# Performance work log

Measured on AMD Instinct MI355X. Metric: run time of the kernel, lower is better.

The kernel has to match this reference:

```python
import jax, jax.numpy as jnp
import numpy as np

W, H = 256, 256          # image width (x) and height (y); image indexed [x, y] like the torch code
N = 8192                 # depth-sorted visible gaussians
TILE = 16                # tile_size default
CHUNK = 128              # gaussians composited per scan step (N % CHUNK == 0)
MIN_WEIGHT = 1e-6        # early-termination threshold from render_pixel


def setup_inputs() -> dict:
    key = jax.random.key(0)
    k1, k2, k3, k4, k5 = jax.random.split(key, 5)
    # pixel-space means, uniformly over the image
    points_xy = jax.random.uniform(k1, (N, 2), dtype=jnp.float32) * jnp.array([W, H], jnp.float32)
    # SPD inverse 2D covariances: Sigma = R diag(var) R^T, inv = R diag(1/var) R^T
    theta = jax.random.uniform(k2, (N,), dtype=jnp.float32) * (2.0 * np.pi)
    sig = jax.random.uniform(k3, (N, 2), dtype=jnp.float32, minval=1.5, maxval=8.0)
    var = sig ** 2
    ct, st = jnp.cos(theta), jnp.sin(theta)
    R = jnp.stack([jnp.stack([ct, -st], -1), jnp.stack([st, ct], -1)], -2)  # [N,2,2]
    inverse_covariance = jnp.einsum('nij,nj,nkj->nik', R, 1.0 / var, R)
    # radius = ceil(2.5 * sqrt(max eigenvalue)) as in compute_radius
    radius = jnp.ceil(2.5 * jnp.sqrt(jnp.max(var, axis=1)))
    colors = jax.random.uniform(k4, (N, 3), dtype=jnp.float32)
    opacity = jax.random.normal(k5, (N,), dtype=jnp.float32)  # pre-sigmoid logits
    return dict(points_xy=points_xy, inverse_covariance=inverse_covariance,
                radius=radius, colors=colors, opacity=opacity)


def _rasterize(points_xy, inverse_covariance, radius, colors, opacity):
    px = jnp.arange(W, dtype=jnp.float32)[:, None]   # [W,1] pixel x coords
    py = jnp.arange(H, dtype=jnp.float32)[None, :]   # [1,H] pixel y coords
    # tile origin for each pixel (tile-based culling as in render_image)
    tile_x0 = ((jnp.arange(W) // TILE) * TILE).astype(jnp.float32)[:, None]  # [W,1]
    tile_y0 = ((jnp.arange(H) // TILE) * TILE).astype(jnp.float32)[None, :]  # [1,H]
    # per-gaussian bounding boxes (preprocess)
    min_x = jnp.floor(points_xy[:, 0] - radius); max_x = jnp.ceil(points_xy[:, 0] + radius)
    min_y = jnp.floor(points_xy[:, 1] - radius); max_y = jnp.ceil(points_xy[:, 1] + radius)

    n_chunks = N // CHUNK
    def chunk(a):
        return a.reshape((n_chunks, CHUNK) + a.shape[1:])
    xs = dict(mx=chunk(points_xy[:, 0]), my=chunk(points_xy[:, 1]),
              a=chunk(inverse_covariance[:, 0, 0]), b=chunk(inverse_covariance[:, 0, 1]),
              c=chunk(inverse_covariance[:, 1, 1]),
              mnx=chunk(min_x), mxx=chunk(max_x), mny=chunk(min_y), mxy=chunk(max_y),
              col=chunk(colors), op=chunk(opacity))

    @jax.checkpoint
    def body(carry, ch):
        T, color = carry  # T: [W,H] remaining transmittance; color: [W,H,3]
        dx = px[None] - ch['mx'][:, None, None]  # [C,W,1]
        dy = py[None] - ch['my'][:, None, None]  # [C,1,H]
        # mahalanobis form d^T Sigma^{-1} d with symmetric inv cov [[a,b],[b,c]]
        q = (ch['a'][:, None, None] * dx * dx
             + 2.0 * ch['b'][:, None, None] * dx * dy
             + ch['c'][:, None, None] * dy * dy)              # [C,W,H]
        alpha = jnp.exp(-0.5 * q) * jax.nn.sigmoid(ch['op'])[:, None, None]
        # gaussian participates for a pixel iff its bbox intersects that pixel's tile
        in_tile = ((ch['mnx'][:, None, None] <= tile_x0[None] + TILE)
                   & (ch['mxx'][:, None, None] >= tile_x0[None])
                   & (ch['mny'][:, None, None] <= tile_y0[None] + TILE)
                   & (ch['mxy'][:, None, None] >= tile_y0[None]))   # [C,W,H]
        alpha = jnp.where(in_tile, alpha, 0.0)
        cum = jnp.cumprod(1.0 - alpha, axis=0)                 # inclusive prefix of (1-alpha)
        T_before = T[None] * jnp.concatenate([jnp.ones_like(cum[:1]), cum[:-1]], axis=0)
        # original: test_weight = T_before*(1-alpha); terminate (skip contribution) if < min_weight
        include = (T[None] * cum) >= MIN_WEIGHT
        contrib = jnp.where(include, T_before * alpha, 0.0)   # [C,W,H]
        color = color + jnp.einsum('cwh,cd->whd', contrib, ch['col'])
        return (T * cum[-1], color), None

    init = (jnp.ones((W, H), jnp.float32), jnp.zeros((W, H, 3), jnp.float32))
    (_, color), _ = jax.lax.scan(body, init, xs)
    return color  # [W,H,3] image indexed [x,y]


def reference(points_xy, inverse_covariance, radius, colors, opacity):
    return _rasterize(points_xy, inverse_covariance, radius, colors, opacity)
```

## Files before the change

### kernel.cpp

```cpp
#include <hip/hip_runtime.h>
#include <hip/hip_fp16.h>

#define WIDTH   256
#define HEIGHT  256
#define NG      8192
#define TILE_SZ 16
#define MINW    1e-6f
#define BLK     1024
#define NBATCH  (NG / BLK)
#define NWAVE   (BLK / 64)
#define NSEG    16
#define RSZ     512
#define KC      (-0.72134752044f)

__global__ __launch_bounds__(256) void prep_kernel(
    const float* __restrict__ pts, const float* __restrict__ icov,
    const float* __restrict__ cols, const float* __restrict__ opac,
    const float* __restrict__ rad,
    float4* __restrict__ table, float4* __restrict__ bbt)
{
    const int g = blockIdx.x * 256 + threadIdx.x;
    const float2 p = ((const float2*)pts)[g];
    const float4 ic = ((const float4*)icov)[g];
    const float r  = rad[g];
    const float op = 1.0f / (1.0f + __expf(-opac[g]));
    const __half2 h = __floats2half2_rn(cols[3 * g], cols[3 * g + 1]);
    unsigned rgbits; __builtin_memcpy(&rgbits, &h, 4);
    table[2 * g + 0] = make_float4(p.x, p.y, KC * ic.x, 2.0f * KC * ic.y);
    table[2 * g + 1] = make_float4(KC * ic.w, op, __uint_as_float(rgbits),
                                   cols[3 * g + 2]);
    bbt[g] = make_float4(floorf(p.x - r), ceilf(p.x + r),
                         floorf(p.y - r), ceilf(p.y + r));
}

__global__ __launch_bounds__(BLK, 4) void raster_kernel(
    const float4* __restrict__ bbt,
    const float4* __restrict__ table,
    float* __restrict__ out)
{
    __shared__ unsigned long long s_ball[NBATCH * NWAVE];
    __shared__ int s_pfx[NBATCH * NWAVE];
    __shared__ __align__(16) char s_pool[32768];
    unsigned short* s_list = (unsigned short*)s_pool;
    float4* s_g = (float4*)(s_pool + 16384);
    __shared__ float s_P[NSEG][256];

    const int tid  = threadIdx.x;
    const int lane = tid & 63;
    const int wave = tid >> 6;
    const int seg  = wave;
    const float tx0 = (float)(blockIdx.x * TILE_SZ);
    const float ty0 = (float)(blockIdx.y * TILE_SZ);
    const float tx1 = tx0 + (float)TILE_SZ;
    const float ty1 = ty0 + (float)TILE_SZ;

    float4 bb[NBATCH];
    #pragma unroll
    for (int b = 0; b < NBATCH; ++b) bb[b] = bbt[b * BLK + tid];
    unsigned int hitbits = 0;
    #pragma unroll
    for (int b = 0; b < NBATCH; ++b) {
        bool hit = (bb[b].x <= tx1) & (bb[b].y >= tx0)
                 & (bb[b].z <= ty1) & (bb[b].w >= ty0);
        unsigned long long m = __ballot(hit);
        if (lane == 0) s_ball[b * NWAVE + wave] = m;
        if (hit) hitbits |= (1u << b);
    }
    __syncthreads();
    if (wave == 0) {
        int v0 = __popcll(s_ball[lane]);
        int v1 = __popcll(s_ball[64 + lane]);
        #pragma unroll
        for (int d = 1; d < 64; d <<= 1) {
            const int t0 = __shfl_up(v0, d);
            const int t1 = __shfl_up(v1, d);
            if (lane >= d) { v0 += t0; v1 += t1; }
        }
        s_pfx[lane] = v0;
        s_pfx[64 + lane] = v1 + __shfl(v0, 63);
    }
    __syncthreads();
    const int count = s_pfx[127];
    {
        unsigned int hb = hitbits;
        const unsigned long long ltmask = (1ull << lane) - 1ull;
        while (hb) {
            const int b = __ffs(hb) - 1;  hb &= hb - 1;
            const int idx = b * NWAVE + wave;
            const unsigned long long m = s_ball[idx];
            const int bs = idx ? s_pfx[idx - 1] : 0;
            s_list[bs + __popcll(m & ltmask)] = (unsigned short)(b * BLK + tid);
        }
    }
    __syncthreads();

    const int q  = tid & 63;
    const int qx = q >> 3, qy = q & 7;
    const float fx = tx0 + (float)(2 * qx);
    const float fy = ty0 + (float)(2 * qy);
    const int p0 = (2 * qx) * 16 + 2 * qy;
    const int pxi[4] = {p0, p0 + 1, p0 + 16, p0 + 17};
    float Tpx = 1.0f;
    float acc[3][4];
    #pragma unroll
    for (int c = 0; c < 3; ++c)
        #pragma unroll
        for (int k = 0; k < 4; ++k) acc[c][k] = 0.0f;

    for (int base = 0; base < count; base += RSZ) {
        const int n = min(RSZ, count - base);
        if (tid < n) {
            const int g = s_list[base + tid];
            s_g[tid * 2 + 0] = table[2 * g + 0];
            s_g[tid * 2 + 1] = table[2 * g + 1];
        }
        __syncthreads();

        const int L  = (n + NSEG - 1) >> 4;
        const int i0 = seg * L;
        const int i1 = min(i0 + L, n);

        float P[4] = {1.f, 1.f, 1.f, 1.f};
        float l[3][4];
        #pragma unroll
        for (int c = 0; c < 3; ++c)
            #pragma unroll
            for (int k = 0; k < 4; ++k) l[c][k] = 0.0f;

        #pragma unroll 2
        for (int i = i0; i < i1; ++i) {
            const float4 g0 = s_g[i * 2 + 0];
            const float4 g1 = s_g[i * 2 + 1];
            const float dya = fy - g0.y,  dyb = dya + 1.0f;
            const float dxa = fx - g0.x,  dxb = dxa + 1.0f;
            const float bya = g0.w * dya, byb = g0.w * dyb;
            const float cya = (g1.x * dya) * dya, cyb = (g1.x * dyb) * dyb;
            const float axa = (g0.z * dxa) * dxa, axb = (g0.z * dxb) * dxb;
            const unsigned rgbits = __float_as_uint(g1.z);
            __half2 h; __builtin_memcpy(&h, &rgbits, 4);
            const float2 rg = __half22float2(h);
            const float qv[4] = { fmaf(dxa, bya, axa + cya),
                                  fmaf(dxa, byb, axa + cyb),
                                  fmaf(dxb, bya, axb + cya),
                                  fmaf(dxb, byb, axb + cyb) };
            #pragma unroll
            for (int k = 0; k < 4; ++k) {
                const float a = g1.y * __builtin_amdgcn_exp2f(qv[k]);
                const float w = P[k] * a;
                l[0][k] = fmaf(w, rg.x, l[0][k]);
                l[1][k] = fmaf(w, rg.y, l[1][k]);
                l[2][k] = fmaf(w, g1.w, l[2][k]);
                P[k] = fmaf(-a, P[k], P[k]);
            }
        }
        #pragma unroll
        for (int k = 0; k < 4; ++k) s_P[seg][pxi[k]] = P[k];
        __syncthreads();

        if (tid < 256) {
            float run = Tpx;
            #pragma unroll
            for (int s = 0; s < NSEG; ++s) {
                const float Pv = s_P[s][tid];
                s_P[s][tid] = run;
                run *= Pv;
            }
            Tpx = run;
        }
        __syncthreads();

        float Tin[4];
        bool gated[4]; bool anyg = false;
        #pragma unroll
        for (int k = 0; k < 4; ++k) {
            Tin[k] = s_P[seg][pxi[k]];
            const bool alive = (Tin[k] >= MINW);
            gated[k] = alive && (Tin[k] * P[k] < MINW);
            if (alive && !gated[k]) {
                acc[0][k] = fmaf(Tin[k], l[0][k], acc[0][k]);
                acc[1][k] = fmaf(Tin[k], l[1][k], acc[1][k]);
                acc[2][k] = fmaf(Tin[k], l[2][k], acc[2][k]);
            }
            anyg |= gated[k];
        }
        if (__ballot(anyg) != 0ull) {
            float Tl[4] = {Tin[0], Tin[1], Tin[2], Tin[3]};
            for (int i = i0; i < i1; ++i) {
                const float4 g0 = s_g[i * 2 + 0];
                const float4 g1 = s_g[i * 2 + 1];
                const float dya = fy - g0.y,  dyb = dya + 1.0f;
                const float dxa = fx - g0.x,  dxb = dxa + 1.0f;
                const float bya = g0.w * dya, byb = g0.w * dyb;
                const float cya = (g1.x * dya) * dya, cyb = (g1.x * dyb) * dyb;
                const float axa = (g0.z * dxa) * dxa, axb = (g0.z * dxb) * dxb;
                const unsigned rgbits = __float_as_uint(g1.z);
                __half2 h; __builtin_memcpy(&h, &rgbits, 4);
                const float2 rg = __half22float2(h);
                const float qv[4] = { fmaf(dxa, bya, axa + cya),
                                      fmaf(dxa, byb, axa + cyb),
                                      fmaf(dxb, bya, axb + cya),
                                      fmaf(dxb, byb, axb + cyb) };
                #pragma unroll
                for (int k = 0; k < 4; ++k) {
                    const float a  = g1.y * __builtin_amdgcn_exp2f(qv[k]);
                    const float Tn = Tl[k] * (1.0f - a);
                    const float w  = (gated[k] && Tn >= MINW) ? Tl[k] * a : 0.0f;
                    acc[0][k] = fmaf(w, rg.x, acc[0][k]);
                    acc[1][k] = fmaf(w, rg.y, acc[1][k]);
                    acc[2][k] = fmaf(w, g1.w, acc[2][k]);
                    Tl[k] = Tn;
                }
            }
        }
        const bool mydead = (tid < 256) ? (Tpx < MINW) : true;
        if (__syncthreads_count(mydead) == BLK) break;
    }

    float sum[3];
    #pragma unroll
    for (int c = 0; c < 3; ++c) {
        __syncthreads();
        #pragma unroll
        for (int k = 0; k < 4; ++k) s_P[seg][pxi[k]] = acc[c][k];
        __syncthreads();
        if (tid < 256) {
            float v = 0.0f;
            #pragma unroll
            for (int s = 0; s < NSEG; ++s) v += s_P[s][tid];
            sum[c] = v;
        }
    }
    if (tid < 256) {
        const int x = blockIdx.x * TILE_SZ + (tid >> 4);
        const int y = blockIdx.y * TILE_SZ + (tid & 15);
        const int o = (x * HEIGHT + y) * 3;
        out[o] = sum[0];  out[o + 1] = sum[1];  out[o + 2] = sum[2];
    }
}

extern "C" void kernel_launch(void* const* d_in, const int* in_sizes, int n_in,
                              void* d_out, int out_size, void* d_ws, size_t ws_size,
                              hipStream_t stream) {
    const float* pts  = (const float*)d_in[0];
    const float* icov = (const float*)d_in[1];
    const float* rad  = (const float*)d_in[2];
    const float* cols = (const float*)d_in[3];
    const float* opac = (const float*)d_in[4];
    float* out = (float*)d_out;
    float4* table = (float4*)d_ws;
    float4* bbt   = table + 2 * NG;
    prep_kernel<<<NG / 256, 256, 0, stream>>>(pts, icov, cols, opac, rad, table, bbt);
    dim3 grid(WIDTH / TILE_SZ, HEIGHT / TILE_SZ);
    raster_kernel<<<grid, dim3(BLK), 0, stream>>>(bbt, table, out);
}
```

Baseline: 78.37 us.

## Fuse prep into raster kernel and split each tile across two blocks

Removes the separate preprocessing kernel: bounding boxes and per-gaussian parameters are now computed directly from the raw inputs inside the raster kernel, saving one launch and the workspace round-trip. Each 16x16 tile is split into two 8x16 halves via a z grid dimension, so each thread handles 2 pixels instead of 4, which doubles the block count and should give more parallelism. The final reduction writes interleaved RGB through shared memory. In exchange, culling and the per-gaussian sigmoid/fp16 packing are recomputed redundantly in every block, twice as many blocks as before.

```diff
diff --git a/kernel.cpp b/kernel.cpp
--- a/kernel.cpp
+++ b/kernel.cpp
@@ -10,32 +10,16 @@
 #define NBATCH  (NG / BLK)
 #define NWAVE   (BLK / 64)
 #define NSEG    16
+#define PXB     128
 #define RSZ     512
 #define KC      (-0.72134752044f)
 
-__global__ __launch_bounds__(256) void prep_kernel(
-    const float* __restrict__ pts, const float* __restrict__ icov,
-    const float* __restrict__ cols, const float* __restrict__ opac,
+__global__ __launch_bounds__(BLK, 8) void raster_kernel(
+    const float* __restrict__ pts,
+    const float* __restrict__ icov,
     const float* __restrict__ rad,
-    float4* __restrict__ table, float4* __restrict__ bbt)
-{
-    const int g = blockIdx.x * 256 + threadIdx.x;
-    const float2 p = ((const float2*)pts)[g];
-    const float4 ic = ((const float4*)icov)[g];
-    const float r  = rad[g];
-    const float op = 1.0f / (1.0f + __expf(-opac[g]));
-    const __half2 h = __floats2half2_rn(cols[3 * g], cols[3 * g + 1]);
-    unsigned rgbits; __builtin_memcpy(&rgbits, &h, 4);
-    table[2 * g + 0] = make_float4(p.x, p.y, KC * ic.x, 2.0f * KC * ic.y);
-    table[2 * g + 1] = make_float4(KC * ic.w, op, __uint_as_float(rgbits),
-                                   cols[3 * g + 2]);
-    bbt[g] = make_float4(floorf(p.x - r), ceilf(p.x + r),
-                         floorf(p.y - r), ceilf(p.y + r));
-}
-
-__global__ __launch_bounds__(BLK, 4) void raster_kernel(
-    const float4* __restrict__ bbt,
-    const float4* __restrict__ table,
+    const float* __restrict__ cols,
+    const float* __restrict__ opac,
     float* __restrict__ out)
 {
     __shared__ unsigned long long s_ball[NBATCH * NWAVE];
@@ -43,7 +27,8 @@
     __shared__ __align__(16) char s_pool[32768];
     unsigned short* s_list = (unsigned short*)s_pool;
     float4* s_g = (float4*)(s_pool + 16384);
-    __shared__ float s_P[NSEG][256];
+    float*  s_red = (float*)s_pool;
+    __shared__ float s_P[NSEG][PXB];
 
     const int tid  = threadIdx.x;
     const int lane = tid & 63;
@@ -54,14 +39,14 @@
     const float tx1 = tx0 + (float)TILE_SZ;
     const float ty1 = ty0 + (float)TILE_SZ;
 
-    float4 bb[NBATCH];
-    #pragma unroll
-    for (int b = 0; b < NBATCH; ++b) bb[b] = bbt[b * BLK + tid];
     unsigned int hitbits = 0;
     #pragma unroll
     for (int b = 0; b < NBATCH; ++b) {
-        bool hit = (bb[b].x <= tx1) & (bb[b].y >= tx0)
-                 & (bb[b].z <= ty1) & (bb[b].w >= ty0);
+        const int g = b * BLK + tid;
+        const float2 p = ((const float2*)pts)[g];
+        const float  r = rad[g];
+        bool hit = (floorf(p.x - r) <= tx1) & (ceilf(p.x + r) >= tx0)
+                 & (floorf(p.y - r) <= ty1) & (ceilf(p.y + r) >= ty0);
         unsigned long long m = __ballot(hit);
         if (lane == 0) s_ball[b * NWAVE + wave] = m;
         if (hit) hitbits |= (1u << b);
@@ -94,25 +79,29 @@
     }
     __syncthreads();
 
-    const int q  = tid & 63;
-    const int qx = q >> 3, qy = q & 7;
-    const float fx = tx0 + (float)(2 * qx);
-    const float fy = ty0 + (float)(2 * qy);
-    const int p0 = (2 * qx) * 16 + 2 * qy;
-    const int pxi[4] = {p0, p0 + 1, p0 + 16, p0 + 17};
+    const int pr = tid & 63;
+    const int xl = pr >> 3, yp = pr & 7;
+    const float fx  = tx0 + (float)(blockIdx.z * 8 + xl);
+    const float fyA = ty0 + (float)(2 * yp);
+    const int pA = xl * 16 + 2 * yp;
+    const int pxi[2] = {pA, pA + 1};
     float Tpx = 1.0f;
-    float acc[3][4];
+    float acc[3][2];
     #pragma unroll
-    for (int c = 0; c < 3; ++c)
-        #pragma unroll
-        for (int k = 0; k < 4; ++k) acc[c][k] = 0.0f;
+    for (int c = 0; c < 3; ++c) { acc[c][0] = 0.0f; acc[c][1] = 0.0f; }
 
     for (int base = 0; base < count; base += RSZ) {
         const int n = min(RSZ, count - base);
         if (tid < n) {
             const int g = s_list[base + tid];
-            s_g[tid * 2 + 0] = table[2 * g + 0];
-            s_g[tid * 2 + 1] = table[2 * g + 1];
+            const float2 p = ((const float2*)pts)[g];
+            const float4 ic = ((const float4*)icov)[g];
+            const float op = 1.0f / (1.0f + __expf(-opac[g]));
+            const __half2 h = __floats2half2_rn(cols[3 * g], cols[3 * g + 1]);
+            unsigned rgbits; __builtin_memcpy(&rgbits, &h, 4);
+            s_g[tid * 2 + 0] = make_float4(p.x, p.y, KC * ic.x, 2.0f * KC * ic.y);
+            s_g[tid * 2 + 1] = make_float4(KC * ic.w, op, __uint_as_float(rgbits),
+                                           cols[3 * g + 2]);
         }
         __syncthreads();
 
@@ -120,31 +109,26 @@
         const int i0 = seg * L;
         const int i1 = min(i0 + L, n);
 
-        float P[4] = {1.f, 1.f, 1.f, 1.f};
-        float l[3][4];
-        #pragma unroll
-        for (int c = 0; c < 3; ++c)
-            #pragma unroll
-            for (int k = 0; k < 4; ++k) l[c][k] = 0.0f;
+        float P[2] = {1.f, 1.f};
+        float l[3][2];
+        #pragma unroll
+        for (int c = 0; c < 3; ++c) { l[c][0] = 0.0f; l[c][1] = 0.0f; }
 
         #pragma unroll 2
         for (int i = i0; i < i1; ++i) {
             const float4 g0 = s_g[i * 2 + 0];
             const float4 g1 = s_g[i * 2 + 1];
-            const float dya = fy - g0.y,  dyb = dya + 1.0f;
-            const float dxa = fx - g0.x,  dxb = dxa + 1.0f;
-            const float bya = g0.w * dya, byb = g0.w * dyb;
-            const float cya = (g1.x * dya) * dya, cyb = (g1.x * dyb) * dyb;
-            const float axa = (g0.z * dxa) * dxa, axb = (g0.z * dxb) * dxb;
+            const float dx  = fx - g0.x;
+            const float axx = (g0.z * dx) * dx;
+            const float bdx = g0.w * dx;
+            const float dyA = fyA - g0.y, dyB = dyA + 1.0f;
+            const float qv[2] = { fmaf(dyA, fmaf(g1.x, dyA, bdx), axx),
+                                  fmaf(dyB, fmaf(g1.x, dyB, bdx), axx) };
             const unsigned rgbits = __float_as_uint(g1.z);
             __half2 h; __builtin_memcpy(&h, &rgbits, 4);
             const float2 rg = __half22float2(h);
-            const float qv[4] = { fmaf(dxa, bya, axa + cya),
-                                  fmaf(dxa, byb, axa + cyb),
-                                  fmaf(dxb, bya, axb + cya),
-                                  fmaf(dxb, byb, axb + cyb) };
             #pragma unroll
-            for (int k = 0; k < 4; ++k) {
+            for (int k = 0; k < 2; ++k) {
                 const float a = g1.y * __builtin_amdgcn_exp2f(qv[k]);
                 const float w = P[k] * a;
                 l[0][k] = fmaf(w, rg.x, l[0][k]);
@@ -153,11 +137,11 @@
                 P[k] = fmaf(-a, P[k], P[k]);
             }
         }
-        #pragma unroll
-        for (int k = 0; k < 4; ++k) s_P[seg][pxi[k]] = P[k];
+        s_P[seg][pxi[0]] = P[0];
+        s_P[seg][pxi[1]] = P[1];
         __syncthreads();
 
-        if (tid < 256) {
+        if (tid < PXB) {
             float run = Tpx;
             #pragma unroll
             for (int s = 0; s < NSEG; ++s) {
@@ -169,10 +153,10 @@
         }
         __syncthreads();
 
-        float Tin[4];
-        bool gated[4]; bool anyg = false;
-        #pragma unroll
-        for (int k = 0; k < 4; ++k) {
+        float Tin[2];
+        bool gated[2]; bool anyg = false;
+        #pragma unroll
+        for (int k = 0; k < 2; ++k) {
             Tin[k] = s_P[seg][pxi[k]];
             const bool alive = (Tin[k] >= MINW);
             gated[k] = alive && (Tin[k] * P[k] < MINW);
@@ -184,24 +168,21 @@
             anyg |= gated[k];
         }
         if (__ballot(anyg) != 0ull) {
-            float Tl[4] = {Tin[0], Tin[1], Tin[2], Tin[3]};
+            float Tl[2] = {Tin[0], Tin[1]};
             for (int i = i0; i < i1; ++i) {
                 const float4 g0 = s_g[i * 2 + 0];
                 const float4 g1 = s_g[i * 2 + 1];
-                const float dya = fy - g0.y,  dyb = dya + 1.0f;
-                const float dxa = fx - g0.x,  dxb = dxa + 1.0f;
-                const float bya = g0.w * dya, byb = g0.w * dyb;
-                const float cya = (g1.x * dya) * dya, cyb = (g1.x * dyb) * dyb;
-                const float axa = (g0.z * dxa) * dxa, axb = (g0.z * dxb) * dxb;
+                const float dx  = fx - g0.x;
+                const float axx = (g0.z * dx) * dx;
+                const float bdx = g0.w * dx;
+                const float dyA = fyA - g0.y, dyB = dyA + 1.0f;
+                const float qv[2] = { fmaf(dyA, fmaf(g1.x, dyA, bdx), axx),
+                                      fmaf(dyB, fmaf(g1.x, dyB, bdx), axx) };
                 const unsigned rgbits = __float_as_uint(g1.z);
                 __half2 h; __builtin_memcpy(&h, &rgbits, 4);
                 const float2 rg = __half22float2(h);
-                const float qv[4] = { fmaf(dxa, bya, axa + cya),
-                                      fmaf(dxa, byb, axa + cyb),
-                                      fmaf(dxb, bya, axb + cya),
-                                      fmaf(dxb, byb, axb + cyb) };
                 #pragma unroll
-                for (int k = 0; k < 4; ++k) {
+                for (int k = 0; k < 2; ++k) {
                     const float a  = g1.y * __builtin_amdgcn_exp2f(qv[k]);
                     const float Tn = Tl[k] * (1.0f - a);
                     const float w  = (gated[k] && Tn >= MINW) ? Tl[k] * a : 0.0f;
@@ -212,29 +193,26 @@
                 }
             }
         }
-        const bool mydead = (tid < 256) ? (Tpx < MINW) : true;
+        const bool mydead = (tid < PXB) ? (Tpx < MINW) : true;
         if (__syncthreads_count(mydead) == BLK) break;
     }
 
-    float sum[3];
     #pragma unroll
-    for (int c = 0; c < 3; ++c) {
-        __syncthreads();
-        #pragma unroll
-        for (int k = 0; k < 4; ++k) s_P[seg][pxi[k]] = acc[c][k];
-        __syncthreads();
-        if (tid < 256) {
-            float v = 0.0f;
-            #pragma unroll
-            for (int s = 0; s < NSEG; ++s) v += s_P[s][tid];
-            sum[c] = v;
-        }
-    }
-    if (tid < 256) {
-        const int x = blockIdx.x * TILE_SZ + (tid >> 4);
-        const int y = blockIdx.y * TILE_SZ + (tid & 15);
-        const int o = (x * HEIGHT + y) * 3;
-        out[o] = sum[0];  out[o + 1] = sum[1];  out[o + 2] = sum[2];
+    for (int k = 0; k < 2; ++k) {
+        s_red[(seg * PXB + pxi[k]) * 3 + 0] = acc[0][k];
+        s_red[(seg * PXB + pxi[k]) * 3 + 1] = acc[1][k];
+        s_red[(seg * PXB + pxi[k]) * 3 + 2] = acc[2][k];
+    }
+    __syncthreads();
+    if (tid < PXB * 3) {
+        const int p  = tid / 3;
+        const int ch = tid - 3 * p;
+        float v = 0.0f;
+        #pragma unroll
+        for (int s = 0; s < NSEG; ++s) v += s_red[(s * PXB + p) * 3 + ch];
+        const int x = blockIdx.x * TILE_SZ + blockIdx.z * 8 + (p >> 4);
+        const int y = blockIdx.y * TILE_SZ + (p & 15);
+        out[(x * HEIGHT + y) * 3 + ch] = v;
     }
 }
 
@@ -247,9 +225,6 @@
     const float* cols = (const float*)d_in[3];
     const float* opac = (const float*)d_in[4];
     float* out = (float*)d_out;
-    float4* table = (float4*)d_ws;
-    float4* bbt   = table + 2 * NG;
-    prep_kernel<<<NG / 256, 256, 0, stream>>>(pts, icov, cols, opac, rad, table, bbt);
-    dim3 grid(WIDTH / TILE_SZ, HEIGHT / TILE_SZ);
-    raster_kernel<<<grid, dim3(BLK), 0, stream>>>(bbt, table, out);
+    dim3 grid(WIDTH / TILE_SZ, HEIGHT / TILE_SZ, 2);
+    raster_kernel<<<grid, dim3(BLK), 0, stream>>>(pts, icov, rad, cols, opac, out);
 }
```

After: 78.10 us (median of 2 runs). About the same (-0.3%).

## Fuse preprocessing into raster kernel and restructure final segment reduction

Applied to the files above, without the earlier changes.

Removes the separate prep kernel launch. The raster kernel now computes bounding boxes and per-gaussian table entries (sigmoid opacity, scaled inverse covariance, half-packed colors) directly from the raw inputs while staging each chunk into shared memory. The cross-segment reduction now makes two passes into the shared pool (half of the waves write, the other half add) and writes all three channels in one coalesced store, replacing three separate reduction rounds. The early-exit barrier is skipped on the last chunk. The cost is redundant per-gaussian preprocessing in each of the 256 blocks and more scattered global loads.

```diff
diff --git a/kernel.cpp b/kernel.cpp
--- a/kernel.cpp
+++ b/kernel.cpp
@@ -13,29 +13,12 @@
 #define RSZ     512
 #define KC      (-0.72134752044f)
 
-__global__ __launch_bounds__(256) void prep_kernel(
-    const float* __restrict__ pts, const float* __restrict__ icov,
-    const float* __restrict__ cols, const float* __restrict__ opac,
+__global__ __launch_bounds__(BLK, 4) void raster_kernel(
+    const float* __restrict__ pts,
+    const float* __restrict__ icov,
     const float* __restrict__ rad,
-    float4* __restrict__ table, float4* __restrict__ bbt)
-{
-    const int g = blockIdx.x * 256 + threadIdx.x;
-    const float2 p = ((const float2*)pts)[g];
-    const float4 ic = ((const float4*)icov)[g];
-    const float r  = rad[g];
-    const float op = 1.0f / (1.0f + __expf(-opac[g]));
-    const __half2 h = __floats2half2_rn(cols[3 * g], cols[3 * g + 1]);
-    unsigned rgbits; __builtin_memcpy(&rgbits, &h, 4);
-    table[2 * g + 0] = make_float4(p.x, p.y, KC * ic.x, 2.0f * KC * ic.y);
-    table[2 * g + 1] = make_float4(KC * ic.w, op, __uint_as_float(rgbits),
-                                   cols[3 * g + 2]);
-    bbt[g] = make_float4(floorf(p.x - r), ceilf(p.x + r),
-                         floorf(p.y - r), ceilf(p.y + r));
-}
-
-__global__ __launch_bounds__(BLK, 4) void raster_kernel(
-    const float4* __restrict__ bbt,
-    const float4* __restrict__ table,
+    const float* __restrict__ cols,
+    const float* __restrict__ opac,
     float* __restrict__ out)
 {
     __shared__ unsigned long long s_ball[NBATCH * NWAVE];
@@ -43,6 +26,7 @@
     __shared__ __align__(16) char s_pool[32768];
     unsigned short* s_list = (unsigned short*)s_pool;
     float4* s_g = (float4*)(s_pool + 16384);
+    float*  pool = (float*)s_pool;
     __shared__ float s_P[NSEG][256];
 
     const int tid  = threadIdx.x;
@@ -54,14 +38,17 @@
     const float tx1 = tx0 + (float)TILE_SZ;
     const float ty1 = ty0 + (float)TILE_SZ;
 
-    float4 bb[NBATCH];
+    float2 pp[NBATCH]; float rr[NBATCH];
     #pragma unroll
-    for (int b = 0; b < NBATCH; ++b) bb[b] = bbt[b * BLK + tid];
+    for (int b = 0; b < NBATCH; ++b) {
+        pp[b] = ((const float2*)pts)[b * BLK + tid];
+        rr[b] = rad[b * BLK + tid];
+    }
     unsigned int hitbits = 0;
     #pragma unroll
     for (int b = 0; b < NBATCH; ++b) {
-        bool hit = (bb[b].x <= tx1) & (bb[b].y >= tx0)
-                 & (bb[b].z <= ty1) & (bb[b].w >= ty0);
+        bool hit = (floorf(pp[b].x - rr[b]) <= tx1) & (ceilf(pp[b].x + rr[b]) >= tx0)
+                 & (floorf(pp[b].y - rr[b]) <= ty1) & (ceilf(pp[b].y + rr[b]) >= ty0);
         unsigned long long m = __ballot(hit);
         if (lane == 0) s_ball[b * NWAVE + wave] = m;
         if (hit) hitbits |= (1u << b);
@@ -111,8 +98,14 @@
         const int n = min(RSZ, count - base);
         if (tid < n) {
             const int g = s_list[base + tid];
-            s_g[tid * 2 + 0] = table[2 * g + 0];
-            s_g[tid * 2 + 1] = table[2 * g + 1];
+            const float2 p = ((const float2*)pts)[g];
+            const float4 ic = ((const float4*)icov)[g];
+            const float op = 1.0f / (1.0f + __expf(-opac[g]));
+            const __half2 h = __floats2half2_rn(cols[3 * g], cols[3 * g + 1]);
+            unsigned rgbits; __builtin_memcpy(&rgbits, &h, 4);
+            s_g[tid * 2 + 0] = make_float4(p.x, p.y, KC * ic.x, 2.0f * KC * ic.y);
+            s_g[tid * 2 + 1] = make_float4(KC * ic.w, op, __uint_as_float(rgbits),
+                                           cols[3 * g + 2]);
         }
         __syncthreads();
 
@@ -212,29 +205,40 @@
                 }
             }
         }
-        const bool mydead = (tid < 256) ? (Tpx < MINW) : true;
-        if (__syncthreads_count(mydead) == BLK) break;
-    }
-
-    float sum[3];
-    #pragma unroll
-    for (int c = 0; c < 3; ++c) {
-        __syncthreads();
-        #pragma unroll
-        for (int k = 0; k < 4; ++k) s_P[seg][pxi[k]] = acc[c][k];
-        __syncthreads();
-        if (tid < 256) {
-            float v = 0.0f;
-            #pragma unroll
-            for (int s = 0; s < NSEG; ++s) v += s_P[s][tid];
-            sum[c] = v;
-        }
-    }
-    if (tid < 256) {
-        const int x = blockIdx.x * TILE_SZ + (tid >> 4);
-        const int y = blockIdx.y * TILE_SZ + (tid & 15);
-        const int o = (x * HEIGHT + y) * 3;
-        out[o] = sum[0];  out[o + 1] = sum[1];  out[o + 2] = sum[2];
+        if (base + RSZ < count) {
+            const bool mydead = (tid < 256) ? (Tpx < MINW) : true;
+            if (__syncthreads_count(mydead) == BLK) break;
+        }
+    }
+    __syncthreads();
+
+    if (seg < 8) {
+        #pragma unroll
+        for (int k = 0; k < 4; ++k) {
+            pool[(seg * 256 + pxi[k]) * 3 + 0] = acc[0][k];
+            pool[(seg * 256 + pxi[k]) * 3 + 1] = acc[1][k];
+            pool[(seg * 256 + pxi[k]) * 3 + 2] = acc[2][k];
+        }
+    }
+    __syncthreads();
+    if (seg >= 8) {
+        #pragma unroll
+        for (int k = 0; k < 4; ++k) {
+            pool[((seg - 8) * 256 + pxi[k]) * 3 + 0] += acc[0][k];
+            pool[((seg - 8) * 256 + pxi[k]) * 3 + 1] += acc[1][k];
+            pool[((seg - 8) * 256 + pxi[k]) * 3 + 2] += acc[2][k];
+        }
+    }
+    __syncthreads();
+    if (tid < 256 * 3) {
+        const int p  = tid / 3;
+        const int ch = tid - 3 * p;
+        float v = 0.0f;
+        #pragma unroll
+        for (int s = 0; s < 8; ++s) v += pool[(s * 256 + p) * 3 + ch];
+        const int x = blockIdx.x * TILE_SZ + (p >> 4);
+        const int y = blockIdx.y * TILE_SZ + (p & 15);
+        out[(x * HEIGHT + y) * 3 + ch] = v;
     }
 }
 
@@ -247,9 +251,6 @@
     const float* cols = (const float*)d_in[3];
     const float* opac = (const float*)d_in[4];
     float* out = (float*)d_out;
-    float4* table = (float4*)d_ws;
-    float4* bbt   = table + 2 * NG;
-    prep_kernel<<<NG / 256, 256, 0, stream>>>(pts, icov, cols, opac, rad, table, bbt);
     dim3 grid(WIDTH / TILE_SZ, HEIGHT / TILE_SZ);
-    raster_kernel<<<grid, dim3(BLK), 0, stream>>>(bbt, table, out);
+    raster_kernel<<<grid, dim3(BLK), 0, stream>>>(pts, icov, rad, cols, opac, out);
 }
```

New measurement: 78.26 us. Within noise of the previous version (-0.1%).
